# Kernel optimization log

Measured on AMD Instinct MI355X. Metric: run time of the kernel, lower is better.

The kernel has to match this reference:

```python
import jax, jax.numpy as jnp
import numpy as np

B, T, F, U, L = 64, 512, 256, 1024, 3
LN_EPS = 1e-12  # tf.contrib.layers.layer_norm default


def setup_inputs() -> dict:
    key = jax.random.key(0)
    ks = jax.random.split(key, 8)

    def w(k, shape):
        return jax.random.normal(k, shape, jnp.float32) / np.float32(np.sqrt(shape[0]))

    return {
        "input": jax.random.normal(ks[0], (B, T, F), jnp.float32),
        "conditioned_lst": jax.random.randint(ks[1], (T,), 0, 2).astype(bool),
        # LSTM layer 0: input = feature F, layers 1..2: input = U
        "W0": w(ks[2], (F + U, 4 * U)), "b0": jnp.zeros((4 * U,), jnp.float32),
        "W1": w(ks[3], (2 * U, 4 * U)), "b1": jnp.zeros((4 * U,), jnp.float32),
        "W2": w(ks[4], (2 * U, 4 * U)), "b2": jnp.zeros((4 * U,), jnp.float32),
        # output dense projection back to feature dim
        "Wd": w(ks[5], (U, F)), "bd": jnp.zeros((F,), jnp.float32),
        # layer norm params
        "gamma": jnp.ones((F,), jnp.float32), "beta": jnp.zeros((F,), jnp.float32),
    }


def _lstm_cell(x, h, c, W, b):
    # BasicLSTMCell: gates in (i, j, f, o) order, forget_bias = 1.0
    z = jnp.dot(jnp.concatenate([x, h], axis=-1), W) + b
    i, j, f, o = jnp.split(z, 4, axis=-1)
    c_new = c * jax.nn.sigmoid(f + 1.0) + jax.nn.sigmoid(i) * jnp.tanh(j)
    h_new = jax.nn.sigmoid(o) * jnp.tanh(c_new)
    return h_new, c_new


def reference(input, conditioned_lst, W0, b0, W1, b1, W2, b2, Wd, bd, gamma, beta):
    Ws, bs = [W0, W1, W2], [b0, b1, b2]
    xs = (jnp.arange(T), jnp.swapaxes(input, 0, 1), conditioned_lst)  # time-major
    carry0 = (jnp.zeros((L, B, U), input.dtype),  # h per layer
              jnp.zeros((L, B, U), input.dtype),  # c per layer
              jnp.zeros((B, F), input.dtype))     # previous emit

    def step(carry, xt):
        hs, cs, prev_emit = carry
        t, x_t, cond_t = xt
        # auto-conditioning: teacher-force on conditioned steps (and step 0)
        x = jnp.where(jnp.logical_or(t == 0, cond_t), x_t, prev_emit)
        new_h, new_c = [], []
        for l in range(L):
            h, c = _lstm_cell(x, hs[l], cs[l], Ws[l], bs[l])
            new_h.append(h)
            new_c.append(c)
            x = h
        y = jnp.dot(x, Wd) + bd  # dense projection [B, F]
        mu = jnp.mean(y, axis=-1, keepdims=True)
        var = jnp.mean(jnp.square(y - mu), axis=-1, keepdims=True)
        y = (y - mu) * jax.lax.rsqrt(var + LN_EPS) * gamma + beta
        emit = jax.nn.relu(y)
        return (jnp.stack(new_h), jnp.stack(new_c), emit), emit

    _, outs = jax.lax.scan(step, carry0, xs)  # [T, B, F]
    return jnp.swapaxes(outs, 0, 1)  # [B, T, F]
```

## Files before the change

kernel.cpp:

```cpp
#include <hip/hip_runtime.h>
#include <math.h>

#define B 64
#define T 512
#define F 256
#define U 1024
#define NBLK 256
#define NTH 512
#define WPAD 68

typedef unsigned short ushort_t;
typedef __attribute__((ext_vector_type(8))) _Float16 f16x8_t;
typedef __attribute__((ext_vector_type(4))) float f32x4_t;

static const size_t OFF_STATS= 0;
static const size_t OFF_COND = 4096;
static const size_t OFF_BAR  = 6144;
static const size_t OFF_H2B  = 7424;
static const size_t OFF_HS   = 269568;
static const size_t OFF_XS   = 1056000;
static const size_t OFF_PW0  = 1088768;
static const size_t OFF_PW1  = 11574528;
static const size_t OFF_PW2  = 28351744;
static const size_t ZERO_BYTES = OFF_PW0;

__device__ __forceinline__ float sigm(float x) {
    return 1.0f / (1.0f + __expf(-x));
}

__device__ __forceinline__ ushort_t f2h(float x) {
    _Float16 h = (_Float16)x;
    union { _Float16 h; ushort_t u; } v; v.h = h;
    return v.u;
}

__device__ __forceinline__ void store_uc_u16(ushort_t* p, ushort_t v) {
    asm volatile("global_store_short %0, %1, off sc0 sc1"
                 :: "v"(p), "v"((unsigned)v) : "memory");
}
__device__ __forceinline__ void store_uc_f32(float* p, float v) {
    asm volatile("global_store_dword %0, %1, off sc0 sc1"
                 :: "v"(p), "v"(v) : "memory");
}
__device__ __forceinline__ void store_uc_b64(void* p, unsigned long long v) {
    asm volatile("global_store_dwordx2 %0, %1, off sc0 sc1"
                 :: "v"(p), "v"(v) : "memory");
}
__device__ __forceinline__ void drain_vmem() {
    asm volatile("s_waitcnt vmcnt(0)" ::: "memory");
}
__device__ __forceinline__ void wait_vm0() {
    asm volatile("s_waitcnt vmcnt(0)" ::: "memory");
    __builtin_amdgcn_sched_barrier(0);
}

__device__ __forceinline__ void phase_sync(int* bar, int epoch, int g) {
    drain_vmem();
    __syncthreads();
    if (threadIdx.x == 0) {
        const int prev = __hip_atomic_fetch_add(bar, 1, __ATOMIC_RELAXED,
                                                __HIP_MEMORY_SCOPE_AGENT);
        if (prev == epoch * NBLK - 1) {
            #pragma unroll
            for (int i = 0; i < 8; ++i)
                __hip_atomic_store(bar + 144 + i * 16, epoch, __ATOMIC_RELAXED,
                                   __HIP_MEMORY_SCOPE_AGENT);
        }
        int* myrelay = bar + 144 + (g & 7) * 16;
        int spins = 0;
        while (__hip_atomic_load(myrelay, __ATOMIC_RELAXED,
                                 __HIP_MEMORY_SCOPE_AGENT) < epoch) {
            __builtin_amdgcn_s_sleep(2);
            if ((++spins & 63) == 0)
                (void)__hip_atomic_load(myrelay, __ATOMIC_ACQUIRE,
                                        __HIP_MEMORY_SCOPE_AGENT);
        }
    }
    __syncthreads();
}

__global__ void prep_kernel(const unsigned char* __restrict__ condraw,
                            const float* __restrict__ input,
                            unsigned char* __restrict__ wsb) {
    __shared__ int s_not_int32;
    const int tid = threadIdx.x;
    if (tid == 0) s_not_int32 = 0;
    __syncthreads();
    if (tid < 512 && (tid & 3) != 0) {
        if (condraw[tid] != 0) s_not_int32 = 1;
    }
    __syncthreads();
    const int is32 = (s_not_int32 == 0);
    int* condw = (int*)(wsb + OFF_COND);
    if (tid < 512) {
        int cv = is32 ? ((const int*)condraw)[tid] : (int)condraw[tid];
        condw[tid] = (cv != 0) ? 1 : 0;
    }
    ushort_t* xs = (ushort_t*)(wsb + OFF_XS);
    for (int i = tid; i < B * F; i += blockDim.x) {
        const int b = i >> 8, f = i & 255;
        xs[(size_t)(((f >> 2) << 6) + b) * 4 + (f & 3)] =
            f2h(input[(size_t)b * (T * F) + f]);
    }
}

__global__ void repack_kernel(const float* __restrict__ W0,
                              const float* __restrict__ W1,
                              const float* __restrict__ W2,
                              unsigned char* __restrict__ wsb) {
    ushort_t* P0 = (ushort_t*)(wsb + OFF_PW0);
    ushort_t* P1 = (ushort_t*)(wsb + OFF_PW1);
    ushort_t* P2 = (ushort_t*)(wsb + OFF_PW2);
    const size_t stride = (size_t)gridDim.x * blockDim.x;
    const size_t tid = (size_t)blockIdx.x * blockDim.x + threadIdx.x;
    const size_t N0 = (size_t)256 * 40 * 512;
    const size_t N12 = (size_t)256 * 64 * 512;
    for (size_t i = tid; i < N0; i += stride) {
        const int g = (int)(i / 20480);
        const int r = (int)(i % 20480);
        const int kt = r >> 9, s = r & 511, L = s >> 3, j = s & 7;
        const int k = kt * 32 + ((L >> 4) << 3) + j;
        const int n = L & 15;
        const int col = ((n >> 2) << 10) + (g << 2) + (n & 3);
        P0[i] = f2h(W0[(size_t)k * 4096 + col]);
    }
    for (size_t i = tid; i < N12; i += stride) {
        const int g = (int)(i / 32768);
        const int r = (int)(i % 32768);
        const int kt = r >> 9, s = r & 511, L = s >> 3, j = s & 7;
        const int k = kt * 32 + ((L >> 4) << 3) + j;
        const int n = L & 15;
        const int col = ((n >> 2) << 10) + (g << 2) + (n & 3);
        const size_t src = (size_t)k * 4096 + col;
        P1[i] = f2h(W1[src]);
        P2[i] = f2h(W2[src]);
    }
}

__global__ void __launch_bounds__(NTH, 2)
lstm_persistent(const float* __restrict__ input,
                const float* __restrict__ b0, const float* __restrict__ b1,
                const float* __restrict__ b2,
                const float* __restrict__ Wd, const float* __restrict__ bd,
                const float* __restrict__ gamma, const float* __restrict__ beta,
                float* __restrict__ out, unsigned char* __restrict__ wsb) {
    const int g = blockIdx.x;
    const int tid = threadIdx.x;
    const int lane = tid & 63;
    const int wv = __builtin_amdgcn_readfirstlane(tid >> 6);
    const int ln15 = lane & 15;
    const int quad = lane >> 4;

    float* h2b = (float*)(wsb + OFF_H2B);
    float* stats = (float*)(wsb + OFF_STATS);
    int* bar = (int*)(wsb + OFF_BAR);
    ushort_t* hs = (ushort_t*)(wsb + OFF_HS);
    ushort_t* xs = (ushort_t*)(wsb + OFF_XS);
    const size_t HSZ = (size_t)256 * 64 * 4;

    __shared__ f16x8_t lds_pw0[40 * 64];
    __shared__ f32x4_t lds_wd4[1024];
    __shared__ float zbuf[128 * WPAD];
    __shared__ int lds_cond[512];

    const int u0 = g << 2;
    const int f0 = g << 2;

    f16x8_t Bw1[8], Bw2[8];
    {
        const ushort_t* p1 = (const ushort_t*)(wsb + OFF_PW1) +
                             (size_t)g * 64 * 512 + (size_t)lane * 8;
        const ushort_t* p2 = (const ushort_t*)(wsb + OFF_PW2) +
                             (size_t)g * 64 * 512 + (size_t)lane * 8;
        #pragma unroll
        for (int i = 0; i < 4; ++i) {
            Bw1[i]     = *(const f16x8_t*)(p1 + (size_t)((wv << 2) + i) * 512);
            Bw1[4 + i] = *(const f16x8_t*)(p1 + (size_t)(32 + (wv << 2) + i) * 512);
            Bw2[i]     = *(const f16x8_t*)(p2 + (size_t)((wv << 2) + i) * 512);
            Bw2[4 + i] = *(const f16x8_t*)(p2 + (size_t)(32 + (wv << 2) + i) * 512);
        }
    }
    {
        const f16x8_t* src = (const f16x8_t*)((const ushort_t*)(wsb + OFF_PW0) +
                                              (size_t)g * 40 * 512);
        for (int i = tid; i < 40 * 64; i += NTH) lds_pw0[i] = src[i];
    }
    if (g < 64) {
        for (int k = tid; k < 1024; k += NTH)
            lds_wd4[k] = *(const f32x4_t*)(Wd + (size_t)k * F + f0);
    }
    for (int i = tid; i < 512; i += NTH) lds_cond[i] = ((const int*)(wsb + OFF_COND))[i];

    const int eb = tid & 63;
    const int eu = (tid >> 6) & 3;

    float bias0[4], bias1[4], bias2[4];
    if (tid < 256) {
        #pragma unroll
        for (int q = 0; q < 4; ++q) {
            bias0[q] = b0[(q << 10) + u0 + eu];
            bias1[q] = b1[(q << 10) + u0 + eu];
            bias2[q] = b2[(q << 10) + u0 + eu];
        }
    }
    float4 gm4 = {0,0,0,0}, bt4 = {0,0,0,0}, bd4 = {0,0,0,0};
    if (g < 64 && wv == 0) {
        gm4 = *(const float4*)(gamma + f0);
        bt4 = *(const float4*)(beta + f0);
        bd4 = *(const float4*)(bd + f0);
    }
    __syncthreads();

    float creg0 = 0.f, creg1 = 0.f, creg2 = 0.f;

    f32x4_t acc0[4], acc1[4], acc2[4];
    #pragma unroll
    for (int mt = 0; mt < 4; ++mt) {
        acc0[mt] = (f32x4_t){0.f, 0.f, 0.f, 0.f};
        acc1[mt] = (f32x4_t){0.f, 0.f, 0.f, 0.f};
        acc2[mt] = (f32x4_t){0.f, 0.f, 0.f, 0.f};
    }

    auto mm4 = [&](f32x4_t (&acc)[4], const ushort_t* base,
                   const f16x8_t (&Bw)[8], const int boff) {
        unsigned long long lo[16], hi[16];
        const char* bb = (const char*)base + (size_t)ln15 * 8 +
                         (size_t)(quad << 1) * 512;
        #pragma unroll
        for (int c = 0; c < 4; ++c) {
            const char* pc = bb + (size_t)((wv << 2) + c) * 4096;
            #pragma unroll
            for (int mt = 0; mt < 4; ++mt) {
                asm volatile("global_load_dwordx2 %0, %1, off sc0 sc1"
                             : "=v"(lo[c * 4 + mt]) : "v"(pc + mt * 128));
                asm volatile("global_load_dwordx2 %0, %1, off sc0 sc1"
                             : "=v"(hi[c * 4 + mt]) : "v"(pc + mt * 128 + 512));
            }
        }
        wait_vm0();
        #pragma unroll
        for (int c = 0; c < 4; ++c) {
            #pragma unroll
            for (int mt = 0; mt < 4; ++mt) {
                union { unsigned long long q[2]; f16x8_t v; } u;
                u.q[0] = lo[c * 4 + mt]; u.q[1] = hi[c * 4 + mt];
                acc[mt] = __builtin_amdgcn_mfma_f32_16x16x32_f16(
                    u.v, Bw[boff + c], acc[mt], 0, 0, 0);
            }
        }
    };

    auto mm_h0 = [&](f32x4_t (&acc)[4], const ushort_t* base) {
        unsigned long long lo[16], hi[16];
        const char* bb = (const char*)base + (size_t)ln15 * 8 +
                         (size_t)(quad << 1) * 512;
        #pragma unroll
        for (int c = 0; c < 4; ++c) {
            const char* pc = bb + (size_t)((wv << 2) + c) * 4096;
            #pragma unroll
            for (int mt = 0; mt < 4; ++mt) {
                asm volatile("global_load_dwordx2 %0, %1, off sc0 sc1"
                             : "=v"(lo[c * 4 + mt]) : "v"(pc + mt * 128));
                asm volatile("global_load_dwordx2 %0, %1, off sc0 sc1"
                             : "=v"(hi[c * 4 + mt]) : "v"(pc + mt * 128 + 512));
            }
        }
        wait_vm0();
        #pragma unroll
        for (int c = 0; c < 4; ++c) {
            const f16x8_t Bb = lds_pw0[(8 + (wv << 2) + c) * 64 + lane];
            #pragma unroll
            for (int mt = 0; mt < 4; ++mt) {
                union { unsigned long long q[2]; f16x8_t v; } u;
                u.q[0] = lo[c * 4 + mt]; u.q[1] = hi[c * 4 + mt];
                acc[mt] = __builtin_amdgcn_mfma_f32_16x16x32_f16(
                    u.v, Bb, acc[mt], 0, 0, 0);
            }
        }
    };

    auto epilogue = [&](f32x4_t (&acc)[4], const float (&bi)[4], float& cr,
                        ushort_t* hdst, float* h2dst) {
        __syncthreads();
        {
            float* zrow = zbuf + (size_t)(wv * 16 + ln15) * WPAD;
            #pragma unroll
            for (int mt = 0; mt < 4; ++mt)
                *(f32x4_t*)(zrow + mt * 16 + (quad << 2)) = acc[mt];
            #pragma unroll
            for (int mt = 0; mt < 4; ++mt) acc[mt] = (f32x4_t){0.f, 0.f, 0.f, 0.f};
        }
        __syncthreads();
        if (tid < 256) {
            float z[4];
            #pragma unroll
            for (int q = 0; q < 4; ++q) {
                float s = bi[q];
                #pragma unroll
                for (int w = 0; w < 8; ++w)
                    s += zbuf[(size_t)(w * 16 + q * 4 + eu) * WPAD + eb];
                z[q] = s;
            }
            const float ig = sigm(z[0]);
            const float gg = tanhf(z[1]);
            const float fg = sigm(z[2] + 1.0f);
            const float og = sigm(z[3]);
            const float cn = cr * fg + ig * gg;
            const float hn = og * tanhf(cn);
            cr = cn;
            store_uc_u16(hdst + ((size_t)g * 64 + eb) * 4 + eu, f2h(hn));
            if (h2dst) store_uc_f32(h2dst + ((size_t)g * 64 + eb) * 4 + eu, hn);
        }
    };

    int epoch = 0;
    for (int t = 0; t < T; ++t) {
        const int p = t & 1;
        const int pn = p ^ 1;
        ushort_t* hs0n = hs + (size_t)(pn * 3 + 0) * HSZ;
        ushort_t* hs1n = hs + (size_t)(pn * 3 + 1) * HSZ;
        ushort_t* hs2n = hs + (size_t)(pn * 3 + 2) * HSZ;

        if (g < 64) {
            mm4(acc1, hs + (size_t)(p * 3 + 1) * HSZ, Bw1, 4);
            mm4(acc2, hs + (size_t)(p * 3 + 2) * HSZ, Bw2, 4);
        }
        {
            unsigned long long xl[4], xh[4];
            const char* bb = (const char*)xs + (size_t)ln15 * 8 +
                             (size_t)(quad << 1) * 512 + (size_t)wv * 4096;
            #pragma unroll
            for (int mt = 0; mt < 4; ++mt) {
                asm volatile("global_load_dwordx2 %0, %1, off sc0 sc1"
                             : "=v"(xl[mt]) : "v"(bb + mt * 128));
                asm volatile("global_load_dwordx2 %0, %1, off sc0 sc1"
                             : "=v"(xh[mt]) : "v"(bb + mt * 128 + 512));
            }
            wait_vm0();
            const f16x8_t Bb = lds_pw0[wv * 64 + lane];
            #pragma unroll
            for (int mt = 0; mt < 4; ++mt) {
                union { unsigned long long q[2]; f16x8_t v; } u;
                u.q[0] = xl[mt]; u.q[1] = xh[mt];
                acc0[mt] = __builtin_amdgcn_mfma_f32_16x16x32_f16(
                    u.v, Bb, acc0[mt], 0, 0, 0);
            }
        }
        epilogue(acc0, bias0, creg0, hs0n, nullptr);
        phase_sync(bar, ++epoch, g);

        mm4(acc1, hs0n, Bw1, 0);
        epilogue(acc1, bias1, creg1, hs1n, nullptr);
        phase_sync(bar, ++epoch, g);

        mm4(acc2, hs1n, Bw2, 0);
        epilogue(acc2, bias2, creg2, hs2n, h2b);
        phase_sync(bar, ++epoch, g);

        if (g < 64) {
            float accd[4] = {0.f, 0.f, 0.f, 0.f};
            #pragma unroll
            for (int half = 0; half < 2; ++half) {
                f32x4_t hv[16];
                const char* hbb = (const char*)h2b +
                    (((size_t)(wv * 32 + half * 16) * 64) + lane) * 16;
                #pragma unroll
                for (int i = 0; i < 16; ++i)
                    asm volatile("global_load_dwordx4 %0, %1, off sc0 sc1"
                                 : "=v"(hv[i]) : "v"(hbb + (size_t)i * 1024));
                wait_vm0();
                #pragma unroll
                for (int i = 0; i < 16; ++i) {
                    const int k = (wv << 7) + (half << 6) + (i << 2);
                    #pragma unroll
                    for (int j = 0; j < 4; ++j) {
                        const f32x4_t w4 = lds_wd4[k + j];
                        accd[0] = fmaf(w4[0], hv[i][j], accd[0]);
                        accd[1] = fmaf(w4[1], hv[i][j], accd[1]);
                        accd[2] = fmaf(w4[2], hv[i][j], accd[2]);
                        accd[3] = fmaf(w4[3], hv[i][j], accd[3]);
                    }
                }
            }
            __syncthreads();
            #pragma unroll
            for (int jj = 0; jj < 4; ++jj)
                zbuf[(size_t)(wv * 16 + jj) * WPAD + lane] = accd[jj];
            __syncthreads();
            if (wv == 0) {
                float yv[4];
                float s = 0.f, ss = 0.f;
                #pragma unroll
                for (int jj = 0; jj < 4; ++jj) {
                    float y = 0.f;
                    #pragma unroll
                    for (int w = 0; w < 8; ++w)
                        y += zbuf[(size_t)(w * 16 + jj) * WPAD + lane];
                    y += (jj == 0) ? bd4.x : (jj == 1) ? bd4.y : (jj == 2) ? bd4.z : bd4.w;
                    yv[jj] = y;
                    s += y;
                    ss += y * y;
                }
                float* st = stats + (size_t)p * (64 * 8);
                atomicAdd(&st[(size_t)lane * 8], s);
                atomicAdd(&st[(size_t)lane * 8 + 1], ss);
                if (lane == 0) {
                    drain_vmem();
                    __hip_atomic_fetch_add(bar + 272, 1, __ATOMIC_RELAXED,
                                           __HIP_MEMORY_SCOPE_AGENT);
                    const int target = (t + 1) * 64;
                    int spins = 0;
                    while (__hip_atomic_load(bar + 272, __ATOMIC_RELAXED,
                                             __HIP_MEMORY_SCOPE_AGENT) < target) {
                        __builtin_amdgcn_s_sleep(2);
                        if ((++spins & 63) == 0)
                            (void)__hip_atomic_load(bar + 272, __ATOMIC_ACQUIRE,
                                                    __HIP_MEMORY_SCOPE_AGENT);
                    }
                }
                union { unsigned long long u64; float f[2]; } sv;
                asm volatile("global_load_dwordx2 %0, %1, off sc0 sc1"
                             : "=v"(sv.u64) : "v"(st + (size_t)lane * 8));
                wait_vm0();
                const float mu = sv.f[0] * (1.0f / F);
                const float var = sv.f[1] * (1.0f / F) - mu * mu;
                const float rs = rsqrtf(var + 1e-12f);
                float em[4];
                em[0] = fmaxf((yv[0] - mu) * rs * gm4.x + bt4.x, 0.0f);
                em[1] = fmaxf((yv[1] - mu) * rs * gm4.y + bt4.y, 0.0f);
                em[2] = fmaxf((yv[2] - mu) * rs * gm4.z + bt4.z, 0.0f);
                em[3] = fmaxf((yv[3] - mu) * rs * gm4.w + bt4.w, 0.0f);
                *(float4*)(out + (size_t)lane * (T * F) + (size_t)t * F + f0) =
                    make_float4(em[0], em[1], em[2], em[3]);
                if (t + 1 < T) {
                    float xn[4];
                    if (lds_cond[t + 1] != 0) {
                        const float4 iv = *(const float4*)(input + (size_t)lane * (T * F) +
                                                           (size_t)(t + 1) * F + f0);
                        xn[0] = iv.x; xn[1] = iv.y; xn[2] = iv.z; xn[3] = iv.w;
                    } else {
                        xn[0] = em[0]; xn[1] = em[1]; xn[2] = em[2]; xn[3] = em[3];
                    }
                    unsigned long long pk =
                        (unsigned long long)f2h(xn[0]) |
                        ((unsigned long long)f2h(xn[1]) << 16) |
                        ((unsigned long long)f2h(xn[2]) << 32) |
                        ((unsigned long long)f2h(xn[3]) << 48);
                    store_uc_b64(xs + ((size_t)g * 64 + lane) * 4, pk);
                }
            }
        } else if (g == 64 && wv == 0) {
            float* st2 = stats + (size_t)pn * (64 * 8);
            store_uc_b64(&st2[(size_t)lane * 8], 0ULL);
        }

        if (t + 1 < T) {
            mm_h0(acc0, hs0n);
            if (g >= 64) {
                mm4(acc1, hs1n, Bw1, 4);
                mm4(acc2, hs2n, Bw2, 4);
            }
        }
        phase_sync(bar, ++epoch, g);
    }
}

extern "C" void kernel_launch(void* const* d_in, const int* in_sizes, int n_in,
                              void* d_out, int out_size, void* d_ws, size_t ws_size,
                              hipStream_t stream) {
    const float* input = (const float*)d_in[0];
    const unsigned char* condraw = (const unsigned char*)d_in[1];
    const float* W0 = (const float*)d_in[2];
    const float* b0 = (const float*)d_in[3];
    const float* W1 = (const float*)d_in[4];
    const float* b1 = (const float*)d_in[5];
    const float* W2 = (const float*)d_in[6];
    const float* b2 = (const float*)d_in[7];
    const float* Wd = (const float*)d_in[8];
    const float* bd = (const float*)d_in[9];
    const float* gamma = (const float*)d_in[10];
    const float* beta = (const float*)d_in[11];
    float* out = (float*)d_out;
    unsigned char* wsb = (unsigned char*)d_ws;

    hipMemsetAsync(d_ws, 0, ZERO_BYTES, stream);
    prep_kernel<<<1, 512, 0, stream>>>(condraw, input, wsb);
    repack_kernel<<<2048, 256, 0, stream>>>(W0, W1, W2, wsb);
    lstm_persistent<<<NBLK, NTH, 0, stream>>>(input, b0, b1, b2, Wd, bd,
                                              gamma, beta, out, wsb);
}
```

Baseline: 25.61 ms.

## Hierarchical grid barrier, cached loads with acquire fence, rebalance h0 recurrent matmul

The grid barrier becomes two-level: blocks count on eight sub-counters, and the last arrival at each sub-counter bumps a master counter, which cuts contention on a single atomic. Inline-asm uncached loads with explicit waits are replaced by plain loads, with an agent-scope acquire fence at the start of each timestep, so the compiler can schedule the loads and they may hit cache. For blocks g<64, the layer-0 recurrent matmul is moved from the dense phase into the layer-1 phase to balance work across phases. Plain cached loads depend on the fence and barrier ordering for coherence across blocks, so stale data is a correctness risk.

```diff
diff --git a/kernel.cpp b/kernel.cpp
--- a/kernel.cpp
+++ b/kernel.cpp
@@ -58,15 +58,20 @@
     drain_vmem();
     __syncthreads();
     if (threadIdx.x == 0) {
-        const int prev = __hip_atomic_fetch_add(bar, 1, __ATOMIC_RELAXED,
-                                                __HIP_MEMORY_SCOPE_AGENT);
-        if (prev == epoch * NBLK - 1) {
-            #pragma unroll
-            for (int i = 0; i < 8; ++i)
-                __hip_atomic_store(bar + 144 + i * 16, epoch, __ATOMIC_RELAXED,
-                                   __HIP_MEMORY_SCOPE_AGENT);
-        }
-        int* myrelay = bar + 144 + (g & 7) * 16;
+        const int sub = g & 7;
+        const int prev = __hip_atomic_fetch_add(bar + sub * 16, 1,
+                                                __ATOMIC_RELAXED, __HIP_MEMORY_SCOPE_AGENT);
+        if (prev == epoch * 32 - 1) {
+            const int pm = __hip_atomic_fetch_add(bar + 128, 1,
+                                                  __ATOMIC_RELAXED, __HIP_MEMORY_SCOPE_AGENT);
+            if (pm == epoch * 8 - 1) {
+                #pragma unroll
+                for (int i = 0; i < 8; ++i)
+                    __hip_atomic_store(bar + 144 + i * 16, epoch, __ATOMIC_RELAXED,
+                                       __HIP_MEMORY_SCOPE_AGENT);
+            }
+        }
+        int* myrelay = bar + 144 + sub * 16;
         int spins = 0;
         while (__hip_atomic_load(myrelay, __ATOMIC_RELAXED,
                                  __HIP_MEMORY_SCOPE_AGENT) < epoch) {
@@ -221,61 +226,52 @@
         acc2[mt] = (f32x4_t){0.f, 0.f, 0.f, 0.f};
     }
 
+    auto ld_frag = [&](const char* p) -> f16x8_t {
+        union { unsigned long long q[2]; f16x8_t v; } u;
+        u.q[0] = *(const unsigned long long*)(p);
+        u.q[1] = *(const unsigned long long*)(p + 512);
+        return u.v;
+    };
+
     auto mm4 = [&](f32x4_t (&acc)[4], const ushort_t* base,
                    const f16x8_t (&Bw)[8], const int boff) {
-        unsigned long long lo[16], hi[16];
+        f16x8_t Ab[4][4];
         const char* bb = (const char*)base + (size_t)ln15 * 8 +
                          (size_t)(quad << 1) * 512;
         #pragma unroll
         for (int c = 0; c < 4; ++c) {
             const char* pc = bb + (size_t)((wv << 2) + c) * 4096;
             #pragma unroll
-            for (int mt = 0; mt < 4; ++mt) {
-                asm volatile("global_load_dwordx2 %0, %1, off sc0 sc1"
-                             : "=v"(lo[c * 4 + mt]) : "v"(pc + mt * 128));
-                asm volatile("global_load_dwordx2 %0, %1, off sc0 sc1"
-                             : "=v"(hi[c * 4 + mt]) : "v"(pc + mt * 128 + 512));
-            }
-        }
-        wait_vm0();
+            for (int mt = 0; mt < 4; ++mt)
+                Ab[c][mt] = ld_frag(pc + mt * 128);
+        }
         #pragma unroll
         for (int c = 0; c < 4; ++c) {
             #pragma unroll
-            for (int mt = 0; mt < 4; ++mt) {
-                union { unsigned long long q[2]; f16x8_t v; } u;
-                u.q[0] = lo[c * 4 + mt]; u.q[1] = hi[c * 4 + mt];
+            for (int mt = 0; mt < 4; ++mt)
                 acc[mt] = __builtin_amdgcn_mfma_f32_16x16x32_f16(
-                    u.v, Bw[boff + c], acc[mt], 0, 0, 0);
-            }
+                    Ab[c][mt], Bw[boff + c], acc[mt], 0, 0, 0);
         }
     };
 
     auto mm_h0 = [&](f32x4_t (&acc)[4], const ushort_t* base) {
-        unsigned long long lo[16], hi[16];
+        f16x8_t Ab[4][4];
         const char* bb = (const char*)base + (size_t)ln15 * 8 +
                          (size_t)(quad << 1) * 512;
         #pragma unroll
         for (int c = 0; c < 4; ++c) {
             const char* pc = bb + (size_t)((wv << 2) + c) * 4096;
             #pragma unroll
-            for (int mt = 0; mt < 4; ++mt) {
-                asm volatile("global_load_dwordx2 %0, %1, off sc0 sc1"
-                             : "=v"(lo[c * 4 + mt]) : "v"(pc + mt * 128));
-                asm volatile("global_load_dwordx2 %0, %1, off sc0 sc1"
-                             : "=v"(hi[c * 4 + mt]) : "v"(pc + mt * 128 + 512));
-            }
-        }
-        wait_vm0();
+            for (int mt = 0; mt < 4; ++mt)
+                Ab[c][mt] = ld_frag(pc + mt * 128);
+        }
         #pragma unroll
         for (int c = 0; c < 4; ++c) {
             const f16x8_t Bb = lds_pw0[(8 + (wv << 2) + c) * 64 + lane];
             #pragma unroll
-            for (int mt = 0; mt < 4; ++mt) {
-                union { unsigned long long q[2]; f16x8_t v; } u;
-                u.q[0] = lo[c * 4 + mt]; u.q[1] = hi[c * 4 + mt];
+            for (int mt = 0; mt < 4; ++mt)
                 acc[mt] = __builtin_amdgcn_mfma_f32_16x16x32_f16(
-                    u.v, Bb, acc[mt], 0, 0, 0);
-            }
+                    Ab[c][mt], Bb, acc[mt], 0, 0, 0);
         }
     };
 
@@ -321,35 +317,30 @@
         ushort_t* hs1n = hs + (size_t)(pn * 3 + 1) * HSZ;
         ushort_t* hs2n = hs + (size_t)(pn * 3 + 2) * HSZ;
 
+        __builtin_amdgcn_fence(__ATOMIC_ACQUIRE, "agent");
+
         if (g < 64) {
             mm4(acc1, hs + (size_t)(p * 3 + 1) * HSZ, Bw1, 4);
             mm4(acc2, hs + (size_t)(p * 3 + 2) * HSZ, Bw2, 4);
         }
         {
-            unsigned long long xl[4], xh[4];
+            f16x8_t Ax[4];
             const char* bb = (const char*)xs + (size_t)ln15 * 8 +
                              (size_t)(quad << 1) * 512 + (size_t)wv * 4096;
             #pragma unroll
-            for (int mt = 0; mt < 4; ++mt) {
-                asm volatile("global_load_dwordx2 %0, %1, off sc0 sc1"
-                             : "=v"(xl[mt]) : "v"(bb + mt * 128));
-                asm volatile("global_load_dwordx2 %0, %1, off sc0 sc1"
-                             : "=v"(xh[mt]) : "v"(bb + mt * 128 + 512));
-            }
-            wait_vm0();
+            for (int mt = 0; mt < 4; ++mt)
+                Ax[mt] = ld_frag(bb + mt * 128);
             const f16x8_t Bb = lds_pw0[wv * 64 + lane];
             #pragma unroll
-            for (int mt = 0; mt < 4; ++mt) {
-                union { unsigned long long q[2]; f16x8_t v; } u;
-                u.q[0] = xl[mt]; u.q[1] = xh[mt];
+            for (int mt = 0; mt < 4; ++mt)
                 acc0[mt] = __builtin_amdgcn_mfma_f32_16x16x32_f16(
-                    u.v, Bb, acc0[mt], 0, 0, 0);
-            }
+                    Ax[mt], Bb, acc0[mt], 0, 0, 0);
         }
         epilogue(acc0, bias0, creg0, hs0n, nullptr);
         phase_sync(bar, ++epoch, g);
 
         mm4(acc1, hs0n, Bw1, 0);
+        if (g < 64) mm_h0(acc0, hs0n);
         epilogue(acc1, bias1, creg1, hs1n, nullptr);
         phase_sync(bar, ++epoch, g);
 
@@ -362,13 +353,11 @@
             #pragma unroll
             for (int half = 0; half < 2; ++half) {
                 f32x4_t hv[16];
-                const char* hbb = (const char*)h2b +
-                    (((size_t)(wv * 32 + half * 16) * 64) + lane) * 16;
+                const f32x4_t* hb4 = (const f32x4_t*)h2b +
+                    (size_t)(wv * 32 + half * 16) * 64 + lane;
                 #pragma unroll
                 for (int i = 0; i < 16; ++i)
-                    asm volatile("global_load_dwordx4 %0, %1, off sc0 sc1"
-                                 : "=v"(hv[i]) : "v"(hbb + (size_t)i * 1024));
-                wait_vm0();
+                    hv[i] = hb4[(size_t)i * 64];
                 #pragma unroll
                 for (int i = 0; i < 16; ++i) {
                     const int k = (wv << 7) + (half << 6) + (i << 2);
@@ -454,12 +443,10 @@
             store_uc_b64(&st2[(size_t)lane * 8], 0ULL);
         }
 
-        if (t + 1 < T) {
+        if (g >= 64 && t + 1 < T) {
             mm_h0(acc0, hs0n);
-            if (g >= 64) {
-                mm4(acc1, hs1n, Bw1, 4);
-                mm4(acc2, hs2n, Bw2, 4);
-            }
+            mm4(acc1, hs1n, Bw1, 4);
+            mm4(acc2, hs2n, Bw2, 4);
         }
         phase_sync(bar, ++epoch, g);
     }
```

After: 24.15 ms. 5.7% less time.
